# Optimization experiments

Hardware: AMD Instinct MI355X
Metric: run time of the kernel (lower is better)

Reference implementation:

```python
import jax, jax.numpy as jnp
import numpy as np

B, T, E, H = 8, 1024, 1024, 16
D = E // H  # head_dim = 64
MAX_SEQ = 4096


def _rope_tables(max_seq_len, head_dim):
    # matches create_rope_lookup: positions 0..max_seq_len-2
    positions = jnp.arange(0, max_seq_len - 1, dtype=jnp.float32)
    inv_freq = 1.0 / (10000.0 ** (jnp.arange(0, head_dim, 2, dtype=jnp.float32) / head_dim))
    freqs = jnp.outer(positions, inv_freq)  # (max_seq_len-1, D//2)
    return jnp.cos(freqs), jnp.sin(freqs)


def setup_inputs() -> dict:
    key = jax.random.key(0)
    k0, k1, k2, k3, k4 = jax.random.split(key, 5)
    x = jax.random.normal(k0, (B, T, E), dtype=jnp.float32)
    w_qkv = jax.random.normal(k1, (3 * E, E), dtype=jnp.float32) * 0.02
    b_qkv = jax.random.normal(k2, (3 * E,), dtype=jnp.float32) * 0.01
    w_out = jax.random.normal(k3, (E, E), dtype=jnp.float32) * 0.02
    b_out = jax.random.normal(k4, (E,), dtype=jnp.float32) * 0.01
    cos_tab, sin_tab = _rope_tables(MAX_SEQ, D)
    return {"x": x, "w_qkv": w_qkv, "b_qkv": b_qkv, "w_out": w_out,
            "b_out": b_out, "cos_tab": cos_tab, "sin_tab": sin_tab}


def _apply_rope(q, k, cos, sin):
    # q,k: (B,H,T,D); cos,sin: (D//2,) -- NOTE: original module indexes the
    # rope table at the single position T (cos_freqs[T,:]), broadcasting the
    # SAME rotation across all sequence positions. Faithfully reproduced.
    def rot(a):
        a_even, a_odd = a[..., ::2], a[..., 1::2]
        r_even = a_even * cos - a_odd * sin
        r_odd = a_even * sin + a_odd * cos
        return jnp.stack([r_even, r_odd], axis=-1).reshape(a.shape)
    return rot(q), rot(k)


def reference(x, w_qkv, b_qkv, w_out, b_out, cos_tab, sin_tab):
    Bb, Tt, Ee = x.shape
    qkv = x @ w_qkv.T + b_qkv  # (B,T,3E)
    q, k, v = jnp.split(qkv, 3, axis=2)
    def heads(a):
        return a.reshape(Bb, Tt, H, D).transpose(0, 2, 1, 3)  # (B,H,T,D)
    q, k, v = heads(q), heads(k), heads(v)
    q, k = _apply_rope(q, k, cos_tab[Tt], sin_tab[Tt])
    scale = 1.0 / jnp.sqrt(jnp.asarray(D, dtype=x.dtype))
    scores = jnp.einsum('bhqd,bhkd->bhqk', q, k) * scale
    causal = jnp.tril(jnp.ones((Tt, Tt), dtype=bool))
    scores = jnp.where(causal, scores, jnp.finfo(scores.dtype).min)
    attn = jax.nn.softmax(scores, axis=-1)
    y = jnp.einsum('bhqk,bhkd->bhqd', attn, v)  # (B,H,T,D)
    y = y.transpose(0, 2, 1, 3).reshape(Bb, Tt, Ee)
    return y @ w_out.T + b_out
```

## Files before the change

kernel.cpp:

```cpp
#include <hip/hip_runtime.h>
#include <hip/hip_bf16.h>
#include <stdint.h>
#include <stddef.h>


typedef __bf16 bf16;
typedef __bf16 bf16x4 __attribute__((ext_vector_type(4)));
typedef __bf16 bf16x8 __attribute__((ext_vector_type(8)));
typedef float  f32x4  __attribute__((ext_vector_type(4)));

#define NEG_BIG (-30000.0f)
#define FIXED_MAX 12.0f

__device__ __forceinline__ void async_cp16(const bf16* g, bf16* l) {
  __builtin_amdgcn_global_load_lds(
      (const __attribute__((address_space(1))) void*)g,
      (__attribute__((address_space(3))) void*)l, 16, 0, 0);
}

__global__ __launch_bounds__(256)
void cvt_f32_bf16(const float* __restrict__ src, bf16* __restrict__ dst, int n8) {
  const int i = blockIdx.x * 256 + threadIdx.x;
  if (i >= n8) return;
  const float4* p = (const float4*)src + (size_t)i * 2;
  const float4 f0 = p[0], f1 = p[1];
  bf16x8 v;
  v[0] = (bf16)f0.x; v[1] = (bf16)f0.y; v[2] = (bf16)f0.z; v[3] = (bf16)f0.w;
  v[4] = (bf16)f1.x; v[5] = (bf16)f1.y; v[6] = (bf16)f1.z; v[7] = (bf16)f1.w;
  ((bf16x8*)dst)[i] = v;
}

__global__ __launch_bounds__(256)
void gemm_qkv(const bf16* __restrict__ A, const bf16* __restrict__ Bw,
              const float* __restrict__ bias,
              bf16* __restrict__ q, bf16* __restrict__ k,
              bf16* __restrict__ vT)
{
  __shared__ bf16 As[128 * 32];
  __shared__ bf16 Bs[128 * 32];
  const int tid  = threadIdx.x;
  const int wave = tid >> 6;
  const int lane = tid & 63;
  const int quad = lane >> 4;
  const int l15  = lane & 15;
  const int wm   = wave >> 1;
  const int wn   = wave & 1;
  const int bm   = blockIdx.y;
  const int bn   = blockIdx.x;
  const int K    = 1024;

  f32x4 acc[4][4];
  const f32x4 fzero = {0.f, 0.f, 0.f, 0.f};
  for (int i = 0; i < 4; i++)
    for (int j = 0; j < 4; j++) acc[i][j] = fzero;

  const int br = lane >> 2;
  const int bc = lane & 3;
  const bf16* Ag0 = A  + (size_t)(bm * 128 + wave * 32 + br) * K + bc * 8;
  const bf16* Ag1 = Ag0 + (size_t)16 * K;
  const bf16* Bg0 = Bw + (size_t)(bn * 128 + wave * 32 + br) * K + bc * 8;
  const bf16* Bg1 = Bg0 + (size_t)16 * K;
  bf16* AsW0 = &As[(wave * 32) * 32];
  bf16* AsW1 = &As[(wave * 32 + 16) * 32];
  bf16* BsW0 = &Bs[(wave * 32) * 32];
  bf16* BsW1 = &Bs[(wave * 32 + 16) * 32];

  for (int kk = 0; kk < K; kk += 32) {
    __syncthreads();
    async_cp16(Ag0 + kk, AsW0);
    async_cp16(Ag1 + kk, AsW1);
    async_cp16(Bg0 + kk, BsW0);
    async_cp16(Bg1 + kk, BsW1);
    __syncthreads();

    bf16x8 af[4], bfr[4];
    for (int mt = 0; mt < 4; mt++)
      af[mt] = *(const bf16x8*)&As[(wm * 64 + mt * 16 + l15) * 32 + quad * 8];
    for (int nt = 0; nt < 4; nt++)
      bfr[nt] = *(const bf16x8*)&Bs[(wn * 64 + nt * 16 + l15) * 32 + quad * 8];
    for (int mt = 0; mt < 4; mt++)
      for (int nt = 0; nt < 4; nt++)
        acc[mt][nt] = __builtin_amdgcn_mfma_f32_16x16x32_bf16(
            af[mt], bfr[nt], acc[mt][nt], 0, 0, 0);
  }

  const int row0 = bm * 128 + wm * 64;
  const int col0 = bn * 128 + wn * 64;
  for (int nt = 0; nt < 4; nt++) {
    const int c  = col0 + nt * 16 + l15;
    const float bv = bias[c];
    if (c < 2048) {
      bf16* dstb = (c < 1024) ? q : k;
      const int hd = c & 1023;
      for (int mt = 0; mt < 4; mt++) {
        const int r = row0 + mt * 16 + quad * 4;
        for (int i = 0; i < 4; i++)
          dstb[(size_t)(r + i) * 1024 + hd] = (bf16)(acc[mt][nt][i] + bv);
      }
    } else {
      const int hh = (c - 2048) >> 6;
      const int d  = (c - 2048) & 63;
      for (int mt = 0; mt < 4; mt++) {
        const int r = row0 + mt * 16 + quad * 4;
        const int bb = r >> 10, t = r & 1023;
        bf16x4 pk;
        for (int i = 0; i < 4; i++) pk[i] = (bf16)(acc[mt][nt][i] + bv);
        *(bf16x4*)&vT[((size_t)(bb * 16 + hh) * 64 + d) * 1024 + t] = pk;
      }
    }
  }
}

__global__ __launch_bounds__(256)
void gemm_out(const bf16* __restrict__ A, const bf16* __restrict__ Bw,
              const float* __restrict__ bias, float* __restrict__ C)
{
  __shared__ bf16 As[128 * 32];
  __shared__ bf16 Bs[128 * 32];
  const int tid  = threadIdx.x;
  const int wave = tid >> 6;
  const int lane = tid & 63;
  const int quad = lane >> 4;
  const int l15  = lane & 15;
  const int wm   = wave >> 1;
  const int wn   = wave & 1;
  const int bm   = blockIdx.y;
  const int bn   = blockIdx.x;
  const int K    = 1024;

  f32x4 acc[4][4];
  const f32x4 fzero = {0.f, 0.f, 0.f, 0.f};
  for (int i = 0; i < 4; i++)
    for (int j = 0; j < 4; j++) acc[i][j] = fzero;

  const int br = lane >> 2;
  const int bc = lane & 3;
  const bf16* Ag0 = A  + (size_t)(bm * 128 + wave * 32 + br) * K + bc * 8;
  const bf16* Ag1 = Ag0 + (size_t)16 * K;
  const bf16* Bg0 = Bw + (size_t)(bn * 128 + wave * 32 + br) * K + bc * 8;
  const bf16* Bg1 = Bg0 + (size_t)16 * K;
  bf16* AsW0 = &As[(wave * 32) * 32];
  bf16* AsW1 = &As[(wave * 32 + 16) * 32];
  bf16* BsW0 = &Bs[(wave * 32) * 32];
  bf16* BsW1 = &Bs[(wave * 32 + 16) * 32];

  for (int kk = 0; kk < K; kk += 32) {
    __syncthreads();
    async_cp16(Ag0 + kk, AsW0);
    async_cp16(Ag1 + kk, AsW1);
    async_cp16(Bg0 + kk, BsW0);
    async_cp16(Bg1 + kk, BsW1);
    __syncthreads();

    bf16x8 af[4], bfr[4];
    for (int mt = 0; mt < 4; mt++)
      af[mt] = *(const bf16x8*)&As[(wm * 64 + mt * 16 + l15) * 32 + quad * 8];
    for (int nt = 0; nt < 4; nt++)
      bfr[nt] = *(const bf16x8*)&Bs[(wn * 64 + nt * 16 + l15) * 32 + quad * 8];
    for (int mt = 0; mt < 4; mt++)
      for (int nt = 0; nt < 4; nt++)
        acc[mt][nt] = __builtin_amdgcn_mfma_f32_16x16x32_bf16(
            af[mt], bfr[nt], acc[mt][nt], 0, 0, 0);
  }

  const int row0 = bm * 128 + wm * 64;
  const int col0 = bn * 128 + wn * 64;
  for (int nt = 0; nt < 4; nt++) {
    const int c  = col0 + nt * 16 + l15;
    const float bv = bias[c];
    for (int mt = 0; mt < 4; mt++) {
      const int r = row0 + mt * 16 + quad * 4;
      for (int i = 0; i < 4; i++)
        C[(size_t)(r + i) * 1024 + c] = acc[mt][nt][i] + bv;
    }
  }
}

__global__ __launch_bounds__(256, 4)
void attn_fused(bf16* __restrict__ qb, const bf16* __restrict__ kb,
                const bf16* __restrict__ vT)
{
  const int pair = blockIdx.x;
  const int bh   = blockIdx.y;
  const int qA = pair;
  const int qB = 15 - pair;
  const int b = bh >> 4;
  const int h = bh & 15;

  __shared__ bf16 Ks[64 * 72];
  __shared__ bf16 Vt[64 * 72];
  __shared__ bf16 Ps[4][16 * 72];

  const int tid  = threadIdx.x;
  const int wave = tid >> 6;
  const int lane = tid & 63;
  const int quad = lane >> 4;
  const int l15  = lane & 15;
  const size_t rowbase = ((size_t)b << 20) + h * 64;
  const size_t vbase   = (size_t)bh << 16;

  bf16x8 qfA[2], qfB[2];
  {
    const int trA = qA * 64 + wave * 16 + l15;
    const int trB = qB * 64 + wave * 16 + l15;
    for (int kf = 0; kf < 2; kf++) {
      const int d0 = kf * 32 + quad * 8;
      bf16x8 a  = *(const bf16x8*)(qb + rowbase + (size_t)trA * 1024 + d0);
      bf16x8 bb = *(const bf16x8*)(qb + rowbase + (size_t)trB * 1024 + d0);
      for (int j = 0; j < 8; j++) {
        qfA[kf][j] = (bf16)((float)a[j] * 0.125f);
        qfB[kf][j] = (bf16)((float)bb[j] * 0.125f);
      }
    }
  }

  const int srow = tid >> 2;
  const int sch  = (tid & 3) * 16;

  f32x4 o_accA[4], o_accB[4];
  const f32x4 fzero = {0.f, 0.f, 0.f, 0.f};
  for (int i = 0; i < 4; i++) { o_accA[i] = fzero; o_accB[i] = fzero; }
  float lA[4] = {0.f, 0.f, 0.f, 0.f};
  float lB[4] = {0.f, 0.f, 0.f, 0.f};

  auto half = [&](int qt, const bf16x8* qf, f32x4* o_acc, float* l_i, int kt) {
    f32x4 s4[4];
    for (int nt = 0; nt < 4; nt++) {
      bf16x8 k0 = *(const bf16x8*)&Ks[(nt * 16 + l15) * 72 + quad * 8];
      bf16x8 k1 = *(const bf16x8*)&Ks[(nt * 16 + l15) * 72 + 32 + quad * 8];
      f32x4 z = fzero;
      z = __builtin_amdgcn_mfma_f32_16x16x32_bf16(qf[0], k0, z, 0, 0, 0);
      z = __builtin_amdgcn_mfma_f32_16x16x32_bf16(qf[1], k1, z, 0, 0, 0);
      s4[nt] = z;
    }
    if (kt == qt) {
      for (int nt = 0; nt < 4; nt++) {
        const int kc = nt * 16 + l15;
        for (int i = 0; i < 4; i++)
          if (kc > wave * 16 + quad * 4 + i) s4[nt][i] = NEG_BIG;
      }
    }
    float p[4][4];
    for (int nt = 0; nt < 4; nt++)
      for (int i = 0; i < 4; i++)
        p[nt][i] = __expf(s4[nt][i] - FIXED_MAX);
    for (int i = 0; i < 4; i++)
      l_i[i] += p[0][i] + p[1][i] + p[2][i] + p[3][i];
    for (int nt = 0; nt < 4; nt++)
      for (int i = 0; i < 4; i++)
        Ps[wave][(quad * 4 + i) * 72 + nt * 16 + l15] = (bf16)p[nt][i];
    bf16x8 pa0 = *(const bf16x8*)&Ps[wave][l15 * 72 + quad * 8];
    bf16x8 pa1 = *(const bf16x8*)&Ps[wave][l15 * 72 + 32 + quad * 8];
    for (int dt = 0; dt < 4; dt++) {
      bf16x8 v0 = *(const bf16x8*)&Vt[(dt * 16 + l15) * 72 + quad * 8];
      bf16x8 v1 = *(const bf16x8*)&Vt[(dt * 16 + l15) * 72 + 32 + quad * 8];
      o_acc[dt] = __builtin_amdgcn_mfma_f32_16x16x32_bf16(pa0, v0, o_acc[dt], 0, 0, 0);
      o_acc[dt] = __builtin_amdgcn_mfma_f32_16x16x32_bf16(pa1, v1, o_acc[dt], 0, 0, 0);
    }
  };

  for (int kt = 0; kt <= qB; kt++) {
    __syncthreads();
    {
      const int kpos = kt * 64 + srow;
      const bf16* kg = kb + rowbase + (size_t)kpos * 1024 + sch;
      *(bf16x8*)&Ks[srow * 72 + sch]     = ((const bf16x8*)kg)[0];
      *(bf16x8*)&Ks[srow * 72 + sch + 8] = ((const bf16x8*)kg)[1];
      const bf16* vg = vT + vbase + (size_t)srow * 1024 + kt * 64 + sch;
      *(bf16x8*)&Vt[srow * 72 + sch]     = ((const bf16x8*)vg)[0];
      *(bf16x8*)&Vt[srow * 72 + sch + 8] = ((const bf16x8*)vg)[1];
    }
    __syncthreads();
    if (kt <= qA) half(qA, qfA, o_accA, lA, kt);
    half(qB, qfB, o_accB, lB, kt);
  }

  for (int i = 0; i < 4; i++) {
    lA[i] += __shfl_xor(lA[i], 1); lA[i] += __shfl_xor(lA[i], 2);
    lA[i] += __shfl_xor(lA[i], 4); lA[i] += __shfl_xor(lA[i], 8);
    lB[i] += __shfl_xor(lB[i], 1); lB[i] += __shfl_xor(lB[i], 2);
    lB[i] += __shfl_xor(lB[i], 4); lB[i] += __shfl_xor(lB[i], 8);
  }

  for (int dt = 0; dt < 4; dt++) {
    for (int i = 0; i < 4; i++) {
      const int d = dt * 16 + l15;
      const int tA = qA * 64 + wave * 16 + quad * 4 + i;
      const int tB = qB * 64 + wave * 16 + quad * 4 + i;
      qb[rowbase + (size_t)tA * 1024 + d] = (bf16)(o_accA[dt][i] / lA[i]);
      qb[rowbase + (size_t)tB * 1024 + d] = (bf16)(o_accB[dt][i] / lB[i]);
    }
  }
}

extern "C" void kernel_launch(void* const* d_in, const int* in_sizes, int n_in,
                              void* d_out, int out_size, void* d_ws, size_t ws_size,
                              hipStream_t stream) {
  int ix = 0, iwq = 1, ibq = 2, iwo = 3, ibo = 4;
  for (int i = 0; i < n_in; i++) {
    switch (in_sizes[i]) {
      case 8388608: ix  = i; break;
      case 3145728: iwq = i; break;
      case 3072:    ibq = i; break;
      case 1048576: iwo = i; break;
      case 1024:    ibo = i; break;
      default: break;
    }
  }
  const float* x     = (const float*)d_in[ix];
  const float* w_qkv = (const float*)d_in[iwq];
  const float* b_qkv = (const float*)d_in[ibq];
  const float* w_out = (const float*)d_in[iwo];
  const float* b_out = (const float*)d_in[ibo];
  float* out = (float*)d_out;

  char* ws = (char*)d_ws;
  bf16* wqb = (bf16*)ws;
  bf16* wob = (bf16*)(ws + 6291456);
  bf16* q   = (bf16*)(ws + 8388608);
  bf16* k   = q + (size_t)8388608;
  bf16* vT  = k + (size_t)8388608;
  bf16* xb = (bf16*)d_out;

  cvt_f32_bf16<<<4096, 256, 0, stream>>>(x, xb, 1048576);
  cvt_f32_bf16<<<1536, 256, 0, stream>>>(w_qkv, wqb, 393216);
  cvt_f32_bf16<<<512,  256, 0, stream>>>(w_out, wob, 131072);

  gemm_qkv<<<dim3(24, 64), dim3(256), 0, stream>>>(xb, wqb, b_qkv, q, k, vT);

  attn_fused<<<dim3(8, 128), dim3(256), 0, stream>>>(q, k, vT);

  gemm_out<<<dim3(8, 64), dim3(256), 0, stream>>>(q, wob, b_out, out);
}
```

Measured before the change: 251.7 us.

## Rewrite QKV GEMM with 256x256 tiles, double-buffered swizzled LDS, pipelined schedule

Replaces the 128x128, single-buffered QKV projection GEMM with a 512-thread kernel that computes 256x256 output tiles using 128KB of dynamic LDS. The A and B tiles are double-buffered and written through a swizzled layout to avoid bank conflicts. Async global-to-LDS copies are interleaved with MFMA phases under explicit waitcnt/barrier control and setprio. The goal is more data reuse per loaded byte and overlap of memory loads with matrix math. The trade-offs are fewer blocks (384 on 256 CUs, so a wave-quantization tail), one block per CU because of LDS size, and higher register pressure.

```diff
diff --git a/kernel.cpp b/kernel.cpp
--- a/kernel.cpp
+++ b/kernel.cpp
@@ -13,6 +13,12 @@
 #define FIXED_MAX 12.0f
 
 __device__ __forceinline__ void async_cp16(const bf16* g, bf16* l) {
+  __builtin_amdgcn_global_load_lds(
+      (const __attribute__((address_space(1))) void*)g,
+      (__attribute__((address_space(3))) void*)l, 16, 0, 0);
+}
+
+__device__ __forceinline__ void cp16(const void* g, void* l) {
   __builtin_amdgcn_global_load_lds(
       (const __attribute__((address_space(1))) void*)g,
       (__attribute__((address_space(3))) void*)l, 16, 0, 0);
@@ -30,86 +36,161 @@
   ((bf16x8*)dst)[i] = v;
 }
 
-__global__ __launch_bounds__(256)
-void gemm_qkv(const bf16* __restrict__ A, const bf16* __restrict__ Bw,
-              const float* __restrict__ bias,
-              bf16* __restrict__ q, bf16* __restrict__ k,
-              bf16* __restrict__ vT)
+#define BAR()   __builtin_amdgcn_s_barrier()
+#define LGKM0() asm volatile("s_waitcnt lgkmcnt(0)" ::: "memory")
+#define VM6()   asm volatile("s_waitcnt vmcnt(6)" ::: "memory")
+
+#define LDA(BUF, MH) do { \
+    const char* _b = sm + (BUF)*32768 + (MH)*16384 + aRow; \
+    _Pragma("unroll") for (int _mt = 0; _mt < 4; _mt++) { \
+      af[_mt][0] = *(const bf16x8*)(_b + _mt*2048 + cb0); \
+      af[_mt][1] = *(const bf16x8*)(_b + _mt*2048 + cb1); } \
+  } while (0)
+
+#define LDB(BUF, NH) do { \
+    const char* _b = sm + 65536 + (BUF)*32768 + (NH)*16384 + bRow; \
+    _Pragma("unroll") for (int _nt = 0; _nt < 2; _nt++) { \
+      bfr[(NH)][_nt][0] = *(const bf16x8*)(_b + _nt*2048 + cb0); \
+      bfr[(NH)][_nt][1] = *(const bf16x8*)(_b + _nt*2048 + cb1); } \
+  } while (0)
+
+#define MM(MH, NH) do { \
+    __builtin_amdgcn_s_setprio(1); \
+    _Pragma("unroll") for (int _mt = 0; _mt < 4; _mt++) { \
+      _Pragma("unroll") for (int _nt = 0; _nt < 2; _nt++) { \
+        acc[(MH)*4+_mt][(NH)*2+_nt] = __builtin_amdgcn_mfma_f32_16x16x32_bf16( \
+            af[_mt][0], bfr[(NH)][_nt][0], acc[(MH)*4+_mt][(NH)*2+_nt], 0, 0, 0); \
+        acc[(MH)*4+_mt][(NH)*2+_nt] = __builtin_amdgcn_mfma_f32_16x16x32_bf16( \
+            af[_mt][1], bfr[(NH)][_nt][1], acc[(MH)*4+_mt][(NH)*2+_nt], 0, 0, 0); } } \
+    __builtin_amdgcn_s_setprio(0); \
+  } while (0)
+
+#define STA(BUF, H, KT) do { if ((KT) < 16) { \
+    const char* _g = (const char*)A + ((H)<<17) + (KT)*128; \
+    char* _s = sm + (BUF)*32768 + (H)*16384 + sOff; \
+    cp16(_g + offA0, _s); cp16(_g + offA1, _s + 1024); } \
+  } while (0)
+
+#define STB(BUF, H, KT) do { if ((KT) < 16) { \
+    const char* _g = (const char*)Bw + ((H)<<16) + (KT)*128; \
+    char* _s = sm + 65536 + (BUF)*32768 + (H)*16384 + sOff; \
+    cp16(_g + offB0, _s); cp16(_g + offB1, _s + 1024); } \
+  } while (0)
+
+__global__ __launch_bounds__(512, 2)
+void gemm_qkv2(const bf16* __restrict__ A, const bf16* __restrict__ Bw,
+               const float* __restrict__ bias,
+               bf16* __restrict__ q, bf16* __restrict__ k2,
+               bf16* __restrict__ vT)
 {
-  __shared__ bf16 As[128 * 32];
-  __shared__ bf16 Bs[128 * 32];
+  extern __shared__ __align__(16) char sm[];
   const int tid  = threadIdx.x;
-  const int wave = tid >> 6;
-  const int lane = tid & 63;
-  const int quad = lane >> 4;
-  const int l15  = lane & 15;
-  const int wm   = wave >> 1;
-  const int wn   = wave & 1;
+  const int w    = tid >> 6;
+  const int l    = tid & 63;
+  const int quad = l >> 4;
+  const int l15  = l & 15;
+  const int wm   = w >> 2;
+  const int wn   = w & 3;
   const int bm   = blockIdx.y;
   const int bn   = blockIdx.x;
-  const int K    = 1024;
-
-  f32x4 acc[4][4];
+
+  const int rj0 = w * 16 + (l >> 3);
+  const int rj1 = rj0 + 8;
+  const int gc  = (l & 7) ^ (l >> 3);
+  const uint32_t offA0 = (uint32_t)(bm*256 + (rj0>>6)*128 + (rj0&63)) * 2048u + (uint32_t)gc*16u;
+  const uint32_t offA1 = (uint32_t)(bm*256 + (rj1>>6)*128 + (rj1&63)) * 2048u + (uint32_t)gc*16u;
+  const uint32_t offB0 = (uint32_t)(bn*256 + (rj0>>5)*64  + (rj0&31)) * 2048u + (uint32_t)gc*16u;
+  const uint32_t offB1 = (uint32_t)(bn*256 + (rj1>>5)*64  + (rj1&31)) * 2048u + (uint32_t)gc*16u;
+  const uint32_t sOff  = (uint32_t)(w*2048 + l*16);
+
+  const int s3 = l15 & 7;
+  const uint32_t cb0  = (uint32_t)(( quad      ^ s3) * 16);
+  const uint32_t cb1  = (uint32_t)(((quad + 4) ^ s3) * 16);
+  const uint32_t aRow = (uint32_t)((wm*64 + l15) * 128);
+  const uint32_t bRow = (uint32_t)((wn*32 + l15) * 128);
+
+  bf16x8 af[4][2];
+  bf16x8 bfr[2][2][2];
+  f32x4 acc[8][4];
   const f32x4 fzero = {0.f, 0.f, 0.f, 0.f};
-  for (int i = 0; i < 4; i++)
+  #pragma unroll
+  for (int i = 0; i < 8; i++)
+    #pragma unroll
     for (int j = 0; j < 4; j++) acc[i][j] = fzero;
 
-  const int br = lane >> 2;
-  const int bc = lane & 3;
-  const bf16* Ag0 = A  + (size_t)(bm * 128 + wave * 32 + br) * K + bc * 8;
-  const bf16* Ag1 = Ag0 + (size_t)16 * K;
-  const bf16* Bg0 = Bw + (size_t)(bn * 128 + wave * 32 + br) * K + bc * 8;
-  const bf16* Bg1 = Bg0 + (size_t)16 * K;
-  bf16* AsW0 = &As[(wave * 32) * 32];
-  bf16* AsW1 = &As[(wave * 32 + 16) * 32];
-  bf16* BsW0 = &Bs[(wave * 32) * 32];
-  bf16* BsW1 = &Bs[(wave * 32 + 16) * 32];
-
-  for (int kk = 0; kk < K; kk += 32) {
-    __syncthreads();
-    async_cp16(Ag0 + kk, AsW0);
-    async_cp16(Ag1 + kk, AsW1);
-    async_cp16(Bg0 + kk, BsW0);
-    async_cp16(Bg1 + kk, BsW1);
-    __syncthreads();
-
-    bf16x8 af[4], bfr[4];
-    for (int mt = 0; mt < 4; mt++)
-      af[mt] = *(const bf16x8*)&As[(wm * 64 + mt * 16 + l15) * 32 + quad * 8];
-    for (int nt = 0; nt < 4; nt++)
-      bfr[nt] = *(const bf16x8*)&Bs[(wn * 64 + nt * 16 + l15) * 32 + quad * 8];
-    for (int mt = 0; mt < 4; mt++)
-      for (int nt = 0; nt < 4; nt++)
-        acc[mt][nt] = __builtin_amdgcn_mfma_f32_16x16x32_bf16(
-            af[mt], bfr[nt], acc[mt][nt], 0, 0, 0);
-  }
-
-  const int row0 = bm * 128 + wm * 64;
-  const int col0 = bn * 128 + wn * 64;
-  for (int nt = 0; nt < 4; nt++) {
-    const int c  = col0 + nt * 16 + l15;
+  STA(0,0,0); STA(0,1,0); STB(0,0,0); STB(0,1,0);
+  STA(1,0,1); STB(1,0,1); STB(1,1,1);
+  VM6(); BAR();
+
+  #pragma unroll 1
+  for (int it2 = 0; it2 < 8; ++it2) {
+    const int t1 = 2*it2 + 1;
+    const int t2 = 2*it2 + 2;
+    const int t3 = 2*it2 + 3;
+    LDA(0,0); LDB(0,0);
+    STA(1,1,t1);
+    BAR(); LGKM0(); MM(0,0); BAR();
+    LDB(0,1);
+    STA(0,0,t2);
+    BAR(); LGKM0(); MM(0,1); BAR();
+    LDA(0,1);
+    STB(0,0,t2);
+    BAR(); LGKM0(); MM(1,0); BAR();
+    STB(0,1,t2);
+    BAR(); MM(1,1); VM6(); BAR();
+    LDA(1,0); LDB(1,0);
+    STA(0,1,t2);
+    BAR(); LGKM0(); MM(0,0); BAR();
+    LDB(1,1);
+    STA(1,0,t3);
+    BAR(); LGKM0(); MM(0,1); BAR();
+    LDA(1,1);
+    STB(1,0,t3);
+    BAR(); LGKM0(); MM(1,0); BAR();
+    STB(1,1,t3);
+    BAR(); MM(1,1); VM6(); BAR();
+  }
+
+  const int row0 = bm*256 + wm*128;
+  const int col0 = bn*256 + wn*64;
+  #pragma unroll
+  for (int fn = 0; fn < 4; fn++) {
+    const int c  = col0 + fn*16 + l15;
     const float bv = bias[c];
     if (c < 2048) {
-      bf16* dstb = (c < 1024) ? q : k;
+      bf16* dstb = (c < 1024) ? q : k2;
       const int hd = c & 1023;
-      for (int mt = 0; mt < 4; mt++) {
-        const int r = row0 + mt * 16 + quad * 4;
+      #pragma unroll
+      for (int fm = 0; fm < 8; fm++) {
+        const int r = row0 + fm*16 + quad*4;
+        #pragma unroll
         for (int i = 0; i < 4; i++)
-          dstb[(size_t)(r + i) * 1024 + hd] = (bf16)(acc[mt][nt][i] + bv);
+          dstb[(size_t)(r + i) * 1024 + hd] = (bf16)(acc[fm][fn][i] + bv);
       }
     } else {
       const int hh = (c - 2048) >> 6;
       const int d  = (c - 2048) & 63;
-      for (int mt = 0; mt < 4; mt++) {
-        const int r = row0 + mt * 16 + quad * 4;
+      #pragma unroll
+      for (int fm = 0; fm < 8; fm++) {
+        const int r = row0 + fm*16 + quad*4;
         const int bb = r >> 10, t = r & 1023;
         bf16x4 pk;
-        for (int i = 0; i < 4; i++) pk[i] = (bf16)(acc[mt][nt][i] + bv);
+        #pragma unroll
+        for (int i = 0; i < 4; i++) pk[i] = (bf16)(acc[fm][fn][i] + bv);
         *(bf16x4*)&vT[((size_t)(bb * 16 + hh) * 64 + d) * 1024 + t] = pk;
       }
     }
   }
 }
+
+#undef LDA
+#undef LDB
+#undef MM
+#undef STA
+#undef STB
+#undef BAR
+#undef LGKM0
+#undef VM6
 
 __global__ __launch_bounds__(256)
 void gemm_out(const bf16* __restrict__ A, const bf16* __restrict__ Bw,
@@ -322,11 +403,18 @@
   bf16* vT  = k + (size_t)8388608;
   bf16* xb = (bf16*)d_out;
 
+  static bool attr_set = false;
+  if (!attr_set) {
+    (void)hipFuncSetAttribute(reinterpret_cast<const void*>(&gemm_qkv2),
+                              hipFuncAttributeMaxDynamicSharedMemorySize, 131072);
+    attr_set = true;
+  }
+
   cvt_f32_bf16<<<4096, 256, 0, stream>>>(x, xb, 1048576);
   cvt_f32_bf16<<<1536, 256, 0, stream>>>(w_qkv, wqb, 393216);
   cvt_f32_bf16<<<512,  256, 0, stream>>>(w_out, wob, 131072);
 
-  gemm_qkv<<<dim3(24, 64), dim3(256), 0, stream>>>(xb, wqb, b_qkv, q, k, vT);
+  gemm_qkv2<<<dim3(12, 32), dim3(512), 131072, stream>>>(xb, wqb, b_qkv, q, k, vT);
 
   attn_fused<<<dim3(8, 128), dim3(256), 0, stream>>>(q, k, vT);
 
```

Result: no change. 255.5 us (+1.5%).

## Double-buffer GEMM K-loop with 64-wide XOR-swizzled LDS tiles

Applied to the files above, without the earlier changes.

Both projection GEMMs now use a 64-element K step, two LDS buffers with the next tile's global-to-LDS copy issued before the current tile's MFMAs, and an XOR swizzle on LDS columns meant to avoid bank conflicts. This halves the number of barrier rounds and overlaps memory loads with compute. LDS use grows to 64 KB per block, which limits occupancy (launch bounds request 2 blocks per CU). There is also one barrier per iteration instead of two.

```diff
diff --git a/kernel.cpp b/kernel.cpp
--- a/kernel.cpp
+++ b/kernel.cpp
@@ -12,7 +12,7 @@
 #define NEG_BIG (-30000.0f)
 #define FIXED_MAX 12.0f
 
-__device__ __forceinline__ void async_cp16(const bf16* g, bf16* l) {
+__device__ __forceinline__ void cp16(const bf16* g, bf16* l) {
   __builtin_amdgcn_global_load_lds(
       (const __attribute__((address_space(1))) void*)g,
       (__attribute__((address_space(3))) void*)l, 16, 0, 0);
@@ -30,80 +30,98 @@
   ((bf16x8*)dst)[i] = v;
 }
 
-__global__ __launch_bounds__(256)
-void gemm_qkv(const bf16* __restrict__ A, const bf16* __restrict__ Bw,
-              const float* __restrict__ bias,
-              bf16* __restrict__ q, bf16* __restrict__ k,
-              bf16* __restrict__ vT)
+#define GEMM3_PROLOGUE()                                                      \
+  const int tid  = threadIdx.x;                                               \
+  const int w    = tid >> 6;                                                  \
+  const int l    = tid & 63;                                                  \
+  const int quad = l >> 4;                                                    \
+  const int l15  = l & 15;                                                    \
+  const int wm   = w >> 1;                                                    \
+  const int wn   = w & 1;                                                     \
+  const int bm   = blockIdx.y;                                                \
+  const int bn   = blockIdx.x;                                                \
+  const int r8   = tid >> 3;                                       \
+  const int gc   = (tid & 7) ^ (r8 & 7);              \
+  const bf16* Ag = A  + (size_t)(bm * 128 + r8) * 1024 + gc * 8;              \
+  const bf16* Bg = Bw + (size_t)(bn * 128 + r8) * 1024 + gc * 8;              \
+  bf16* AsD = &As[0][0] + r8 * 64 + (tid & 7) * 8;                            \
+  bf16* BsD = &Bs[0][0] + r8 * 64 + (tid & 7) * 8;                            \
+  const int s3   = l15 & 7;                                                   \
+  const int arow = (wm * 64 + l15) * 64;                                      \
+  const int brow = (wn * 64 + l15) * 64;                                      \
+  f32x4 acc[4][4];                                                            \
+  const f32x4 fzero = {0.f, 0.f, 0.f, 0.f};                                   \
+  _Pragma("unroll") for (int i = 0; i < 4; i++)                               \
+    _Pragma("unroll") for (int j = 0; j < 4; j++) acc[i][j] = fzero;
+
+#define GEMM3_STAGE(d, kt) do {                                               \
+    _Pragma("unroll") for (int o = 0; o < 4; o++) {                           \
+      cp16(Ag + (size_t)o * 32768 + (kt) * 64, AsD + (d) * 8192 + o * 2048);  \
+      cp16(Bg + (size_t)o * 32768 + (kt) * 64, BsD + (d) * 8192 + o * 2048);  \
+    }                                                                         \
+  } while (0)
+
+#define GEMM3_KLOOP() do {                                                    \
+    GEMM3_STAGE(0, 0);                                                        \
+    __syncthreads();                                                          \
+    _Pragma("unroll 1")                                                       \
+    for (int kt = 0; kt < 16; ++kt) {                                         \
+      const int cur = kt & 1;                                                 \
+      if (kt < 15) GEMM3_STAGE(cur ^ 1, kt + 1);                              \
+      bf16x8 af[2][4], bfr[2][4];                                             \
+      _Pragma("unroll") for (int ks = 0; ks < 2; ks++)                        \
+        _Pragma("unroll") for (int mt = 0; mt < 4; mt++)                      \
+          af[ks][mt] = *(const bf16x8*)&As[cur][arow + mt * 1024 +            \
+                                              (((ks * 4 + quad) ^ s3) * 8)];  \
+      _Pragma("unroll") for (int ks = 0; ks < 2; ks++)                        \
+        _Pragma("unroll") for (int nt = 0; nt < 4; nt++)                      \
+          bfr[ks][nt] = *(const bf16x8*)&Bs[cur][brow + nt * 1024 +           \
+                                              (((ks * 4 + quad) ^ s3) * 8)];  \
+      _Pragma("unroll") for (int ks = 0; ks < 2; ks++)                        \
+        _Pragma("unroll") for (int mt = 0; mt < 4; mt++)                      \
+          _Pragma("unroll") for (int nt = 0; nt < 4; nt++)                    \
+            acc[mt][nt] = __builtin_amdgcn_mfma_f32_16x16x32_bf16(            \
+                af[ks][mt], bfr[ks][nt], acc[mt][nt], 0, 0, 0);               \
+      __syncthreads();                                                        \
+    }                                                                         \
+  } while (0)
+
+__global__ __launch_bounds__(256, 2)
+void gemm_qkv3(const bf16* __restrict__ A, const bf16* __restrict__ Bw,
+               const float* __restrict__ bias,
+               bf16* __restrict__ q, bf16* __restrict__ k2,
+               bf16* __restrict__ vT)
 {
-  __shared__ bf16 As[128 * 32];
-  __shared__ bf16 Bs[128 * 32];
-  const int tid  = threadIdx.x;
-  const int wave = tid >> 6;
-  const int lane = tid & 63;
-  const int quad = lane >> 4;
-  const int l15  = lane & 15;
-  const int wm   = wave >> 1;
-  const int wn   = wave & 1;
-  const int bm   = blockIdx.y;
-  const int bn   = blockIdx.x;
-  const int K    = 1024;
-
-  f32x4 acc[4][4];
-  const f32x4 fzero = {0.f, 0.f, 0.f, 0.f};
-  for (int i = 0; i < 4; i++)
-    for (int j = 0; j < 4; j++) acc[i][j] = fzero;
-
-  const int br = lane >> 2;
-  const int bc = lane & 3;
-  const bf16* Ag0 = A  + (size_t)(bm * 128 + wave * 32 + br) * K + bc * 8;
-  const bf16* Ag1 = Ag0 + (size_t)16 * K;
-  const bf16* Bg0 = Bw + (size_t)(bn * 128 + wave * 32 + br) * K + bc * 8;
-  const bf16* Bg1 = Bg0 + (size_t)16 * K;
-  bf16* AsW0 = &As[(wave * 32) * 32];
-  bf16* AsW1 = &As[(wave * 32 + 16) * 32];
-  bf16* BsW0 = &Bs[(wave * 32) * 32];
-  bf16* BsW1 = &Bs[(wave * 32 + 16) * 32];
-
-  for (int kk = 0; kk < K; kk += 32) {
-    __syncthreads();
-    async_cp16(Ag0 + kk, AsW0);
-    async_cp16(Ag1 + kk, AsW1);
-    async_cp16(Bg0 + kk, BsW0);
-    async_cp16(Bg1 + kk, BsW1);
-    __syncthreads();
-
-    bf16x8 af[4], bfr[4];
-    for (int mt = 0; mt < 4; mt++)
-      af[mt] = *(const bf16x8*)&As[(wm * 64 + mt * 16 + l15) * 32 + quad * 8];
-    for (int nt = 0; nt < 4; nt++)
-      bfr[nt] = *(const bf16x8*)&Bs[(wn * 64 + nt * 16 + l15) * 32 + quad * 8];
-    for (int mt = 0; mt < 4; mt++)
-      for (int nt = 0; nt < 4; nt++)
-        acc[mt][nt] = __builtin_amdgcn_mfma_f32_16x16x32_bf16(
-            af[mt], bfr[nt], acc[mt][nt], 0, 0, 0);
-  }
+  __shared__ bf16 As[2][128 * 64];
+  __shared__ bf16 Bs[2][128 * 64];
+  GEMM3_PROLOGUE();
+  GEMM3_KLOOP();
 
   const int row0 = bm * 128 + wm * 64;
   const int col0 = bn * 128 + wn * 64;
+  #pragma unroll
   for (int nt = 0; nt < 4; nt++) {
     const int c  = col0 + nt * 16 + l15;
     const float bv = bias[c];
     if (c < 2048) {
-      bf16* dstb = (c < 1024) ? q : k;
+      bf16* dstb = (c < 1024) ? q : k2;
       const int hd = c & 1023;
+      #pragma unroll
       for (int mt = 0; mt < 4; mt++) {
         const int r = row0 + mt * 16 + quad * 4;
+        #pragma unroll
         for (int i = 0; i < 4; i++)
           dstb[(size_t)(r + i) * 1024 + hd] = (bf16)(acc[mt][nt][i] + bv);
       }
     } else {
       const int hh = (c - 2048) >> 6;
       const int d  = (c - 2048) & 63;
+      #pragma unroll
       for (int mt = 0; mt < 4; mt++) {
         const int r = row0 + mt * 16 + quad * 4;
         const int bb = r >> 10, t = r & 1023;
         bf16x4 pk;
+        #pragma unroll
         for (int i = 0; i < 4; i++) pk[i] = (bf16)(acc[mt][nt][i] + bv);
         *(bf16x4*)&vT[((size_t)(bb * 16 + hh) * 64 + d) * 1024 + t] = pk;
       }
@@ -111,65 +129,25 @@
   }
 }
 
-__global__ __launch_bounds__(256)
-void gemm_out(const bf16* __restrict__ A, const bf16* __restrict__ Bw,
-              const float* __restrict__ bias, float* __restrict__ C)
+__global__ __launch_bounds__(256, 2)
+void gemm_out3(const bf16* __restrict__ A, const bf16* __restrict__ Bw,
+               const float* __restrict__ bias, float* __restrict__ C)
 {
-  __shared__ bf16 As[128 * 32];
-  __shared__ bf16 Bs[128 * 32];
-  const int tid  = threadIdx.x;
-  const int wave = tid >> 6;
-  const int lane = tid & 63;
-  const int quad = lane >> 4;
-  const int l15  = lane & 15;
-  const int wm   = wave >> 1;
-  const int wn   = wave & 1;
-  const int bm   = blockIdx.y;
-  const int bn   = blockIdx.x;
-  const int K    = 1024;
-
-  f32x4 acc[4][4];
-  const f32x4 fzero = {0.f, 0.f, 0.f, 0.f};
-  for (int i = 0; i < 4; i++)
-    for (int j = 0; j < 4; j++) acc[i][j] = fzero;
-
-  const int br = lane >> 2;
-  const int bc = lane & 3;
-  const bf16* Ag0 = A  + (size_t)(bm * 128 + wave * 32 + br) * K + bc * 8;
-  const bf16* Ag1 = Ag0 + (size_t)16 * K;
-  const bf16* Bg0 = Bw + (size_t)(bn * 128 + wave * 32 + br) * K + bc * 8;
-  const bf16* Bg1 = Bg0 + (size_t)16 * K;
-  bf16* AsW0 = &As[(wave * 32) * 32];
-  bf16* AsW1 = &As[(wave * 32 + 16) * 32];
-  bf16* BsW0 = &Bs[(wave * 32) * 32];
-  bf16* BsW1 = &Bs[(wave * 32 + 16) * 32];
-
-  for (int kk = 0; kk < K; kk += 32) {
-    __syncthreads();
-    async_cp16(Ag0 + kk, AsW0);
-    async_cp16(Ag1 + kk, AsW1);
-    async_cp16(Bg0 + kk, BsW0);
-    async_cp16(Bg1 + kk, BsW1);
-    __syncthreads();
-
-    bf16x8 af[4], bfr[4];
-    for (int mt = 0; mt < 4; mt++)
-      af[mt] = *(const bf16x8*)&As[(wm * 64 + mt * 16 + l15) * 32 + quad * 8];
-    for (int nt = 0; nt < 4; nt++)
-      bfr[nt] = *(const bf16x8*)&Bs[(wn * 64 + nt * 16 + l15) * 32 + quad * 8];
-    for (int mt = 0; mt < 4; mt++)
-      for (int nt = 0; nt < 4; nt++)
-        acc[mt][nt] = __builtin_amdgcn_mfma_f32_16x16x32_bf16(
-            af[mt], bfr[nt], acc[mt][nt], 0, 0, 0);
-  }
+  __shared__ bf16 As[2][128 * 64];
+  __shared__ bf16 Bs[2][128 * 64];
+  GEMM3_PROLOGUE();
+  GEMM3_KLOOP();
 
   const int row0 = bm * 128 + wm * 64;
   const int col0 = bn * 128 + wn * 64;
+  #pragma unroll
   for (int nt = 0; nt < 4; nt++) {
     const int c  = col0 + nt * 16 + l15;
     const float bv = bias[c];
+    #pragma unroll
     for (int mt = 0; mt < 4; mt++) {
       const int r = row0 + mt * 16 + quad * 4;
+      #pragma unroll
       for (int i = 0; i < 4; i++)
         C[(size_t)(r + i) * 1024 + c] = acc[mt][nt][i] + bv;
     }
@@ -326,9 +304,9 @@
   cvt_f32_bf16<<<1536, 256, 0, stream>>>(w_qkv, wqb, 393216);
   cvt_f32_bf16<<<512,  256, 0, stream>>>(w_out, wob, 131072);
 
-  gemm_qkv<<<dim3(24, 64), dim3(256), 0, stream>>>(xb, wqb, b_qkv, q, k, vT);
+  gemm_qkv3<<<dim3(24, 64), dim3(256), 0, stream>>>(xb, wqb, b_qkv, q, k, vT);
 
   attn_fused<<<dim3(8, 128), dim3(256), 0, stream>>>(q, k, vT);
 
-  gemm_out<<<dim3(8, 64), dim3(256), 0, stream>>>(q, wob, b_out, out);
-}
+  gemm_out3<<<dim3(8, 64), dim3(256), 0, stream>>>(q, wob, b_out, out);
+}
```

Result: faster. 241.9 us (-3.9%).

## Double-buffer LDS in both GEMMs with XOR-swizzled layout and deeper K tile

Applied to the files above, without the earlier changes.

Both projection GEMMs now double-buffer their LDS tiles, so the global-to-LDS copy for the next K step is issued before the MFMAs of the current step, with one barrier per iteration instead of two. The LDS column slot is XOR-swizzled by row to reduce bank conflicts on the fragment reads. The output GEMM also doubles its K tile to 64, halving the iteration count. The cost is more LDS per block, which caps occupancy, and the new launch bounds fix it at 5 and 2 blocks per CU.

```diff
diff --git a/kernel.cpp b/kernel.cpp
--- a/kernel.cpp
+++ b/kernel.cpp
@@ -12,7 +12,7 @@
 #define NEG_BIG (-30000.0f)
 #define FIXED_MAX 12.0f
 
-__device__ __forceinline__ void async_cp16(const bf16* g, bf16* l) {
+__device__ __forceinline__ void cp16(const bf16* g, bf16* l) {
   __builtin_amdgcn_global_load_lds(
       (const __attribute__((address_space(1))) void*)g,
       (__attribute__((address_space(3))) void*)l, 16, 0, 0);
@@ -30,80 +30,98 @@
   ((bf16x8*)dst)[i] = v;
 }
 
-__global__ __launch_bounds__(256)
-void gemm_qkv(const bf16* __restrict__ A, const bf16* __restrict__ Bw,
-              const float* __restrict__ bias,
-              bf16* __restrict__ q, bf16* __restrict__ k,
-              bf16* __restrict__ vT)
+__global__ __launch_bounds__(256, 5)
+void gemm_qkv3(const bf16* __restrict__ A, const bf16* __restrict__ Bw,
+               const float* __restrict__ bias,
+               bf16* __restrict__ q, bf16* __restrict__ k2,
+               bf16* __restrict__ vT)
 {
-  __shared__ bf16 As[128 * 32];
-  __shared__ bf16 Bs[128 * 32];
+  __shared__ bf16 As[2][128 * 32];
+  __shared__ bf16 Bs[2][128 * 32];
   const int tid  = threadIdx.x;
-  const int wave = tid >> 6;
-  const int lane = tid & 63;
-  const int quad = lane >> 4;
-  const int l15  = lane & 15;
-  const int wm   = wave >> 1;
-  const int wn   = wave & 1;
+  const int w    = tid >> 6;
+  const int l    = tid & 63;
+  const int quad = l >> 4;
+  const int l15  = l & 15;
+  const int wm   = w >> 1;
+  const int wn   = w & 1;
   const int bm   = blockIdx.y;
   const int bn   = blockIdx.x;
-  const int K    = 1024;
+
+  const int r4 = tid >> 2;
+  const int gc = (tid & 3) ^ (r4 & 3);
+  const bf16* Ag = A  + (size_t)(bm * 128 + r4) * 1024 + gc * 8;
+  const bf16* Bg = Bw + (size_t)(bn * 128 + r4) * 1024 + gc * 8;
+  bf16* AsD = &As[0][0] + r4 * 32 + (tid & 3) * 8;
+  bf16* BsD = &Bs[0][0] + r4 * 32 + (tid & 3) * 8;
+
+  const int s2   = l15 & 3;
+  const int arow = (wm * 64 + l15) * 32;
+  const int brow = (wn * 64 + l15) * 32;
+  const int rslot = (quad ^ s2) * 8;
 
   f32x4 acc[4][4];
   const f32x4 fzero = {0.f, 0.f, 0.f, 0.f};
+  #pragma unroll
   for (int i = 0; i < 4; i++)
+    #pragma unroll
     for (int j = 0; j < 4; j++) acc[i][j] = fzero;
 
-  const int br = lane >> 2;
-  const int bc = lane & 3;
-  const bf16* Ag0 = A  + (size_t)(bm * 128 + wave * 32 + br) * K + bc * 8;
-  const bf16* Ag1 = Ag0 + (size_t)16 * K;
-  const bf16* Bg0 = Bw + (size_t)(bn * 128 + wave * 32 + br) * K + bc * 8;
-  const bf16* Bg1 = Bg0 + (size_t)16 * K;
-  bf16* AsW0 = &As[(wave * 32) * 32];
-  bf16* AsW1 = &As[(wave * 32 + 16) * 32];
-  bf16* BsW0 = &Bs[(wave * 32) * 32];
-  bf16* BsW1 = &Bs[(wave * 32 + 16) * 32];
-
-  for (int kk = 0; kk < K; kk += 32) {
-    __syncthreads();
-    async_cp16(Ag0 + kk, AsW0);
-    async_cp16(Ag1 + kk, AsW1);
-    async_cp16(Bg0 + kk, BsW0);
-    async_cp16(Bg1 + kk, BsW1);
-    __syncthreads();
-
+  #define QKV_STAGE(d, kt) do {                                               \
+      _Pragma("unroll") for (int o = 0; o < 2; o++) {                         \
+        cp16(Ag + (size_t)o * 65536 + (kt) * 32, AsD + (d) * 4096 + o * 2048);\
+        cp16(Bg + (size_t)o * 65536 + (kt) * 32, BsD + (d) * 4096 + o * 2048);\
+      }                                                                       \
+    } while (0)
+
+  QKV_STAGE(0, 0);
+  __syncthreads();
+  #pragma unroll 1
+  for (int kt = 0; kt < 32; ++kt) {
+    const int cur = kt & 1;
+    if (kt < 31) QKV_STAGE(cur ^ 1, kt + 1);
     bf16x8 af[4], bfr[4];
+    #pragma unroll
     for (int mt = 0; mt < 4; mt++)
-      af[mt] = *(const bf16x8*)&As[(wm * 64 + mt * 16 + l15) * 32 + quad * 8];
+      af[mt] = *(const bf16x8*)&As[cur][arow + mt * 512 + rslot];
+    #pragma unroll
     for (int nt = 0; nt < 4; nt++)
-      bfr[nt] = *(const bf16x8*)&Bs[(wn * 64 + nt * 16 + l15) * 32 + quad * 8];
+      bfr[nt] = *(const bf16x8*)&Bs[cur][brow + nt * 512 + rslot];
+    #pragma unroll
     for (int mt = 0; mt < 4; mt++)
+      #pragma unroll
       for (int nt = 0; nt < 4; nt++)
         acc[mt][nt] = __builtin_amdgcn_mfma_f32_16x16x32_bf16(
             af[mt], bfr[nt], acc[mt][nt], 0, 0, 0);
-  }
+    __syncthreads();
+  }
+  #undef QKV_STAGE
 
   const int row0 = bm * 128 + wm * 64;
   const int col0 = bn * 128 + wn * 64;
+  #pragma unroll
   for (int nt = 0; nt < 4; nt++) {
     const int c  = col0 + nt * 16 + l15;
     const float bv = bias[c];
     if (c < 2048) {
-      bf16* dstb = (c < 1024) ? q : k;
+      bf16* dstb = (c < 1024) ? q : k2;
       const int hd = c & 1023;
+      #pragma unroll
       for (int mt = 0; mt < 4; mt++) {
         const int r = row0 + mt * 16 + quad * 4;
+        #pragma unroll
         for (int i = 0; i < 4; i++)
           dstb[(size_t)(r + i) * 1024 + hd] = (bf16)(acc[mt][nt][i] + bv);
       }
     } else {
       const int hh = (c - 2048) >> 6;
       const int d  = (c - 2048) & 63;
+      #pragma unroll
       for (int mt = 0; mt < 4; mt++) {
         const int r = row0 + mt * 16 + quad * 4;
         const int bb = r >> 10, t = r & 1023;
         bf16x4 pk;
+        #pragma unroll
         for (int i = 0; i < 4; i++) pk[i] = (bf16)(acc[mt][nt][i] + bv);
         *(bf16x4*)&vT[((size_t)(bb * 16 + hh) * 64 + d) * 1024 + t] = pk;
       }
@@ -111,65 +129,85 @@
   }
 }
 
-__global__ __launch_bounds__(256)
-void gemm_out(const bf16* __restrict__ A, const bf16* __restrict__ Bw,
-              const float* __restrict__ bias, float* __restrict__ C)
+__global__ __launch_bounds__(256, 2)
+void gemm_out3(const bf16* __restrict__ A, const bf16* __restrict__ Bw,
+               const float* __restrict__ bias, float* __restrict__ C)
 {
-  __shared__ bf16 As[128 * 32];
-  __shared__ bf16 Bs[128 * 32];
+  __shared__ bf16 As[2][128 * 64];
+  __shared__ bf16 Bs[2][128 * 64];
   const int tid  = threadIdx.x;
-  const int wave = tid >> 6;
-  const int lane = tid & 63;
-  const int quad = lane >> 4;
-  const int l15  = lane & 15;
-  const int wm   = wave >> 1;
-  const int wn   = wave & 1;
+  const int w    = tid >> 6;
+  const int l    = tid & 63;
+  const int quad = l >> 4;
+  const int l15  = l & 15;
+  const int wm   = w >> 1;
+  const int wn   = w & 1;
   const int bm   = blockIdx.y;
   const int bn   = blockIdx.x;
-  const int K    = 1024;
-
+  const int r8   = tid >> 3;
+  const int gc   = (tid & 7) ^ (r8 & 7);
+  const bf16* Ag = A  + (size_t)(bm * 128 + r8) * 1024 + gc * 8;
+  const bf16* Bg = Bw + (size_t)(bn * 128 + r8) * 1024 + gc * 8;
+  bf16* AsD = &As[0][0] + r8 * 64 + (tid & 7) * 8;
+  bf16* BsD = &Bs[0][0] + r8 * 64 + (tid & 7) * 8;
+  const int s3   = l15 & 7;
+  const int arow = (wm * 64 + l15) * 64;
+  const int brow = (wn * 64 + l15) * 64;
   f32x4 acc[4][4];
   const f32x4 fzero = {0.f, 0.f, 0.f, 0.f};
+  #pragma unroll
   for (int i = 0; i < 4; i++)
+    #pragma unroll
     for (int j = 0; j < 4; j++) acc[i][j] = fzero;
 
-  const int br = lane >> 2;
-  const int bc = lane & 3;
-  const bf16* Ag0 = A  + (size_t)(bm * 128 + wave * 32 + br) * K + bc * 8;
-  const bf16* Ag1 = Ag0 + (size_t)16 * K;
-  const bf16* Bg0 = Bw + (size_t)(bn * 128 + wave * 32 + br) * K + bc * 8;
-  const bf16* Bg1 = Bg0 + (size_t)16 * K;
-  bf16* AsW0 = &As[(wave * 32) * 32];
-  bf16* AsW1 = &As[(wave * 32 + 16) * 32];
-  bf16* BsW0 = &Bs[(wave * 32) * 32];
-  bf16* BsW1 = &Bs[(wave * 32 + 16) * 32];
-
-  for (int kk = 0; kk < K; kk += 32) {
+  #define OUT_STAGE(d, kt) do {                                               \
+      _Pragma("unroll") for (int o = 0; o < 4; o++) {                         \
+        cp16(Ag + (size_t)o * 32768 + (kt) * 64, AsD + (d) * 8192 + o * 2048);\
+        cp16(Bg + (size_t)o * 32768 + (kt) * 64, BsD + (d) * 8192 + o * 2048);\
+      }                                                                       \
+    } while (0)
+
+  OUT_STAGE(0, 0);
+  __syncthreads();
+  #pragma unroll 1
+  for (int kt = 0; kt < 16; ++kt) {
+    const int cur = kt & 1;
+    if (kt < 15) OUT_STAGE(cur ^ 1, kt + 1);
+    bf16x8 af[2][4], bfr[2][4];
+    #pragma unroll
+    for (int ks = 0; ks < 2; ks++)
+      #pragma unroll
+      for (int mt = 0; mt < 4; mt++)
+        af[ks][mt] = *(const bf16x8*)&As[cur][arow + mt * 1024 +
+                                             (((ks * 4 + quad) ^ s3) * 8)];
+    #pragma unroll
+    for (int ks = 0; ks < 2; ks++)
+      #pragma unroll
+      for (int nt = 0; nt < 4; nt++)
+        bfr[ks][nt] = *(const bf16x8*)&Bs[cur][brow + nt * 1024 +
+                                              (((ks * 4 + quad) ^ s3) * 8)];
+    #pragma unroll
+    for (int ks = 0; ks < 2; ks++)
+      #pragma unroll
+      for (int mt = 0; mt < 4; mt++)
+        #pragma unroll
+        for (int nt = 0; nt < 4; nt++)
+          acc[mt][nt] = __builtin_amdgcn_mfma_f32_16x16x32_bf16(
+              af[ks][mt], bfr[ks][nt], acc[mt][nt], 0, 0, 0);
     __syncthreads();
-    async_cp16(Ag0 + kk, AsW0);
-    async_cp16(Ag1 + kk, AsW1);
-    async_cp16(Bg0 + kk, BsW0);
-    async_cp16(Bg1 + kk, BsW1);
-    __syncthreads();
-
-    bf16x8 af[4], bfr[4];
-    for (int mt = 0; mt < 4; mt++)
-      af[mt] = *(const bf16x8*)&As[(wm * 64 + mt * 16 + l15) * 32 + quad * 8];
-    for (int nt = 0; nt < 4; nt++)
-      bfr[nt] = *(const bf16x8*)&Bs[(wn * 64 + nt * 16 + l15) * 32 + quad * 8];
-    for (int mt = 0; mt < 4; mt++)
-      for (int nt = 0; nt < 4; nt++)
-        acc[mt][nt] = __builtin_amdgcn_mfma_f32_16x16x32_bf16(
-            af[mt], bfr[nt], acc[mt][nt], 0, 0, 0);
-  }
+  }
+  #undef OUT_STAGE
 
   const int row0 = bm * 128 + wm * 64;
   const int col0 = bn * 128 + wn * 64;
+  #pragma unroll
   for (int nt = 0; nt < 4; nt++) {
     const int c  = col0 + nt * 16 + l15;
     const float bv = bias[c];
+    #pragma unroll
     for (int mt = 0; mt < 4; mt++) {
       const int r = row0 + mt * 16 + quad * 4;
+      #pragma unroll
       for (int i = 0; i < 4; i++)
         C[(size_t)(r + i) * 1024 + c] = acc[mt][nt][i] + bv;
     }
@@ -326,9 +364,9 @@
   cvt_f32_bf16<<<1536, 256, 0, stream>>>(w_qkv, wqb, 393216);
   cvt_f32_bf16<<<512,  256, 0, stream>>>(w_out, wob, 131072);
 
-  gemm_qkv<<<dim3(24, 64), dim3(256), 0, stream>>>(xb, wqb, b_qkv, q, k, vT);
+  gemm_qkv3<<<dim3(24, 64), dim3(256), 0, stream>>>(xb, wqb, b_qkv, q, k, vT);
 
   attn_fused<<<dim3(8, 128), dim3(256), 0, stream>>>(q, k, vT);
 
-  gemm_out<<<dim3(8, 64), dim3(256), 0, stream>>>(q, wob, b_out, out);
-}
+  gemm_out3<<<dim3(8, 64), dim3(256), 0, stream>>>(q, wob, b_out, out);
+}
```

Result: no change. 253.3 us (+0.6%).
